# Kernel optimization log

Measured on AMD Instinct MI355X. Metric: run time of the kernel, lower is better.

The kernel has to match this reference:

```python
import jax, jax.numpy as jnp
import numpy as np
import math

LOG_2PI = math.log(2.0 * math.pi)
MIN_CLIP, MAX_CLIP = -5.0, 5.0


def _lse(x, axis):
    return jax.nn.logsumexp(x, axis=axis)


def _gaussian_multi(m1, v1, m2, v2):
    # product of two diagonal Gaussians in log-std parameterization
    v1s = jnp.exp(2.0 * v1)
    v2s = jnp.exp(2.0 * v2)
    add = v1s + v2s
    la = jnp.log(add)
    scale = (-0.5 * (LOG_2PI + la + (m1 - m2) ** 2 / add)).sum(-1)
    mu = (m1 * v2s + m2 * v1s) / add
    var = v1 + v2 - 0.5 * la
    return scale, mu, var


def _energy(sents, mask, tw, tpm, tpv, tcm, tcv, sw_tab, sm_tab, sv_tab):
    B, T = sents.shape
    L, _, TC = tw.shape
    G = tpm.shape[-1]
    EC = sw_tab.shape[1] // L
    clip = lambda x: jnp.clip(x, MIN_CLIP, MAX_CLIP)
    s_mu = clip(sm_tab[sents].reshape(B, T, 1, L, 1, EC, G))
    s_var = clip(sv_tab[sents].reshape(B, T, 1, L, 1, EC, G))
    s_w = sw_tab[sents].reshape(B, T, 1, L, 1, EC)
    t_w = tw.reshape(1, 1, 1, L, L, 1, 1, TC)
    t_p_mu = clip(tpm.reshape(1, 1, 1, L, L, 1, 1, TC, G))
    t_p_var = clip(tpv.reshape(1, 1, 1, L, L, 1, 1, TC, G))
    t_c_mu = clip(tcm.reshape(1, 1, L, L, TC, 1, G))
    t_c_var = clip(tcv.reshape(1, 1, L, L, TC, 1, G))
    cs_scale, cs_mu, cs_var = _gaussian_multi(s_mu, s_var, t_c_mu, t_c_var)
    cs_scale = cs_scale + s_w  # (B,T,L,L,TC,EC)
    # parent-child fusion over consecutive timesteps -> (B,T-1,L,L,L,TC,EC,TC)
    csp, _, _ = _gaussian_multi(jnp.expand_dims(cs_mu[:, :-1], (4, 7)),
                                jnp.expand_dims(cs_var[:, :-1], (4, 7)),
                                t_p_mu, t_p_var)
    mask1 = mask[:, 1:].reshape(B, T - 1, 1, 1, 1, 1, 1, 1)
    csp = csp * mask1 + jnp.expand_dims(cs_scale[:, :-1], (4, 7)) + t_w * mask1
    last = jnp.broadcast_to(jnp.expand_dims(cs_scale[:, -1:], (4, 7)),
                            (B, 1, L, L, L, TC, EC, TC))
    energy = jnp.concatenate([csp, last], axis=1)
    return energy * mask.reshape(B, T, 1, 1, 1, 1, 1, 1)


def _loss(sents, target, mask, tw, tpm, tpv, tcm, tcv, sw_tab, sm_tab, sv_tab):
    B, T = sents.shape
    L, _, TC = tw.shape
    energy = _energy(sents, mask, tw, tpm, tpv, tcm, tcv, sw_tab, sm_tab, sv_tab)
    e_t = jnp.moveaxis(energy, 1, 0)  # (T,B,L,L,L,TC,EC,TC)
    tgt_t = target.T                  # (T,B)
    tgt_next = jnp.concatenate([tgt_t[1:], jnp.zeros((1, B), tgt_t.dtype)], axis=0)
    mask_t = mask.T                   # (T,B)
    bidx = jnp.arange(B)
    # t = 0 : root label is L-1
    e0 = e_t[0]
    part = _lse(_lse(e0[:, -1], axis=4), axis=3)  # (B,L,L,TC)
    tmp0 = e0[bidx, jnp.full((B,), L - 1), tgt_t[0], tgt_next[0]]  # (B,TC,EC,TC)
    tgt_e = _lse(_lse(tmp0, axis=2), axis=1)      # (B,TC) (initial tgt_energy is zeros)

    def step(carry, xs):
        part, tgt_e = carry
        e, tg, tn, pv, m = xs
        pn = _lse(_lse(_lse(e + part[:, :, :, None, :, None, None], 5), 4), 1)
        part = part + (pn - part) * m[:, None, None, None]
        tmp = e[bidx, pv, tg, tn]  # (B,TC,EC,TC)
        te_new = _lse(_lse(tmp + tgt_e[:, :, None, None], 2), 1)
        tgt_e = tgt_e + (te_new - tgt_e) * m[:, None]
        return (part, tgt_e), None

    (part, tgt_e), _ = jax.lax.scan(
        step, (part, tgt_e),
        (e_t[1:], tgt_t[1:], tgt_next[1:], tgt_t[:-1], mask_t[1:]))
    part = part.mean(axis=2)  # (B,L,TC)
    loss = _lse(_lse(part, 2), 1) - _lse(tgt_e, 1)
    return loss.mean()


def setup_inputs() -> dict:
    key = jax.random.key(0)
    ks = jax.random.split(key, 10)
    V, NL, G, TC, EC = 50000, 45, 1, 1, 1
    L = NL + 1
    B, T = 4, 96

    def xavier(k, shape):
        rf = int(np.prod(shape[2:])) if len(shape) > 2 else 1
        fan_in = shape[1] * rf
        fan_out = shape[0] * rf
        std = math.sqrt(2.0 / (fan_in + fan_out))
        return jax.random.normal(k, shape, jnp.float32) * std

    return {
        "sents": jax.random.randint(ks[0], (B, T), 0, V, dtype=jnp.int32),
        "target": jax.random.randint(ks[1], (B, T), 0, NL, dtype=jnp.int32),
        "mask": jnp.ones((B, T), jnp.float32),
        "trans_weight": xavier(ks[2], (L, L, TC)),
        "trans_p_mu": xavier(ks[3], (L, L, TC, G)),
        "trans_p_var": xavier(ks[4], (L, L, TC, G)),
        "trans_c_mu": xavier(ks[5], (L, L, TC, G)),
        "trans_c_var": xavier(ks[6], (L, L, TC, G)),
        "s_weight_tab": jax.random.normal(ks[7], (V, L * EC), jnp.float32),
        "s_mu_tab": jax.random.normal(ks[8], (V, L * G * EC), jnp.float32),
        "s_var_tab": jax.random.normal(ks[9], (V, L * G * EC), jnp.float32),
    }


def reference(sents, target, mask, trans_weight, trans_p_mu, trans_p_var,
              trans_c_mu, trans_c_var, s_weight_tab, s_mu_tab, s_var_tab):
    return _loss(sents, target, mask, trans_weight, trans_p_mu, trans_p_var,
                 trans_c_mu, trans_c_var, s_weight_tab, s_mu_tab, s_var_tab)
```

## Files before the change

### kernel.cpp

```cpp
#include <hip/hip_runtime.h>
#include <hip/hip_fp16.h>
#include <math.h>

#define L 46
#define LSQ 2116
#define T 96
#define B 4
#define WROWH_U32 24
#define KSTRIDE_U32 25600
#define LOG_2PI 1.8378770664093453f
#define LN2f 0.6931471805599453f
#define LN2_EXP 8.2629582e-8f
#define INV_LN2 1.4426950408889634f

typedef float v2f __attribute__((ext_vector_type(2)));

__device__ __forceinline__ float clip5(float x) {
    return fminf(fmaxf(x, -5.0f), 5.0f);
}

__device__ __forceinline__ unsigned fxform(float f) {
    unsigned u = __float_as_uint(f);
    return (u & 0x80000000u) ? ~u : (u | 0x80000000u);
}
__device__ __forceinline__ float funxform(unsigned u) {
    return __uint_as_float((u & 0x80000000u) ? (u ^ 0x80000000u) : ~u);
}

__device__ __forceinline__ float bitlog(float x) {
    return (float)(int)(__float_as_uint(x) - 0x3f800000u) * LN2_EXP;
}

__device__ __forceinline__ v2f bfpair(unsigned u) {
    v2f r;
    r.x = __uint_as_float(u << 16);
    r.y = __uint_as_float(u & 0xFFFF0000u);
    return r;
}
__device__ __forceinline__ unsigned short f2bf(float f) {
    return (unsigned short)((__float_as_uint(f) + 0x8000u) >> 16);
}

#define BARRIER_LGKM() asm volatile("s_waitcnt lgkmcnt(0)\n\ts_barrier" ::: "memory")

__device__ __forceinline__ unsigned enc_e4m3_sw(float f) {
    if (!(f >= 0.0f)) return 0u;
    if (f < 0.015625f) {
        int m = (int)rintf(f * 512.0f);
        return (unsigned)m;
    }
    unsigned u = __float_as_uint(fminf(f, 448.0f));
    int e = (int)((u >> 23) & 255) - 127;
    int mant = (int)((u >> 20) & 7) + (int)((u >> 19) & 1);
    int Eb = e + 7;
    if (mant == 8) { mant = 0; ++Eb; }
    if (Eb > 15) { Eb = 15; mant = 6; }
    return (unsigned)((Eb << 3) | mant);
}
template <bool HI>
__device__ __forceinline__ unsigned enc_pk(float a, float b, unsigned old) {
#if __has_builtin(__builtin_amdgcn_cvt_pk_fp8_f32)
    return (unsigned)__builtin_amdgcn_cvt_pk_fp8_f32(a, b, (int)old, HI);
#else
    unsigned lo = enc_e4m3_sw(a) | (enc_e4m3_sw(b) << 8);
    return HI ? ((old & 0x0000FFFFu) | (lo << 16)) : ((old & 0xFFFF0000u) | lo);
#endif
}

__device__ __forceinline__ float dec1_sw(unsigned b) {
    int e = (b >> 3) & 15, m = b & 7;
    return e ? ldexpf((float)(8 + m), e - 10) : ldexpf((float)m, -9);
}
template <bool HI>
__device__ __forceinline__ v2f dec_pk(unsigned u) {
#if __has_builtin(__builtin_amdgcn_cvt_pk_f32_fp8)
    return __builtin_amdgcn_cvt_pk_f32_fp8(u, HI);
#else
    unsigned x = HI ? (u >> 16) : u;
    v2f r; r.x = dec1_sw(x & 0xffu); r.y = dec1_sw((x >> 8) & 0xffu);
    return r;
#endif
}

__device__ __forceinline__ void dp_acc(v2f& acc, unsigned kv, v2f wA, v2f wB) {
    acc += dec_pk<false>(kv) * wA;
    acc += dec_pk<true>(kv)  * wB;
}

__global__ __launch_bounds__(1024) void build_kernel(
    const int*   __restrict__ sents,
    const int*   __restrict__ target,
    const float* __restrict__ tw,
    const float* __restrict__ tpm,
    const float* __restrict__ tpv,
    const float* __restrict__ tcm,
    const float* __restrict__ tcv,
    const float* __restrict__ sw_tab,
    const float* __restrict__ sm_tab,
    const float* __restrict__ sv_tab,
    unsigned* __restrict__ K8,
    float*    __restrict__ escB,
    float*    __restrict__ psD,
    float*    __restrict__ P0,
    float*    __restrict__ tgtc,
    unsigned* __restrict__ done)
{
    __shared__ float sPS[LSQ], sW2[LSQ], sTP[LSQ];
    __shared__ float sW1T[L][48];
    __shared__ float sMUT[L][48];
    const int bt = blockIdx.x;
    const int t  = bt % T;
    const int b  = bt / T;
    const int sent = sents[bt];

    if (bt == 0 && threadIdx.x == 0) *done = 0u;

    if (threadIdx.x < L * 2) {
        int r = threadIdx.x >> 1, c = 46 + (threadIdx.x & 1);
        sW1T[r][c] = __uint_as_float(0x7f800000u);
        sMUT[r][c] = 0.0f;
    }

    for (int i = threadIdx.x; i < LSQ; i += 1024) {
        sW2[i] = __expf(2.0f * clip5(tpv[i]));
        sTP[i] = clip5(tpm[i]);
        int bb = i % L;
        int aa = i / L;
        float smu  = clip5(sm_tab[sent * L + bb]);
        float svar = clip5(sv_tab[sent * L + bb]);
        float sw   = sw_tab[sent * L + bb];
        float tc_m = clip5(tcm[i]);
        float tc_v = clip5(tcv[i]);
        float v1s = __expf(2.0f * svar);
        float v2s = __expf(2.0f * tc_v);
        float add = v1s + v2s;
        float inv = __builtin_amdgcn_rcpf(add);
        float la  = __logf(add);
        float d   = smu - tc_m;
        float psv = fmaf(-0.5f, LOG_2PI + la + d * d * inv, sw);
        sPS[i] = psv;
        psD[(size_t)bt * LSQ + i] = psv;
        sMUT[bb][aa] = (smu * v2s + tc_m * v1s) * inv;
        sW1T[bb][aa] = v1s * v2s * inv;
    }
    __syncthreads();

    if (threadIdx.x == 0) {
        const int* tg = target + b * T;
        float contrib;
        if (t == 0) {
            int i2 = tg[0] * L + tg[1];
            float ad = sW1T[tg[0]][45] + sW2[i2];
            float d  = sMUT[tg[0]][45] - sTP[i2];
            contrib = sPS[45 * L + tg[0]] + tw[i2]
                    - 0.5f * (LOG_2PI + __logf(ad) + d * d * __builtin_amdgcn_rcpf(ad));
        } else if (t == T - 1) {
            contrib = sPS[tg[T - 2] * L + tg[T - 1]];
        } else {
            int i2 = tg[t] * L + tg[t + 1];
            float ad = sW1T[tg[t]][tg[t - 1]] + sW2[i2];
            float d  = sMUT[tg[t]][tg[t - 1]] - sTP[i2];
            contrib = sPS[tg[t - 1] * L + tg[t]] + tw[i2]
                    - 0.5f * (LOG_2PI + __logf(ad) + d * d * __builtin_amdgcn_rcpf(ad));
        }
        tgtc[bt] = contrib;
    }

    if (t == 0) {
        for (int oi = threadIdx.x; oi < LSQ; oi += 1024) {
            int bb = oi / L;
            float ad = sW1T[bb][45] + sW2[oi];
            float d  = sMUT[bb][45] - sTP[oi];
            P0[b * LSQ + oi] = sPS[45 * L + bb] + tw[oi]
                - 0.5f * (LOG_2PI + __logf(ad) + d * d * __builtin_amdgcn_rcpf(ad));
        }
        return;
    }
    if (t == T - 1) return;

    unsigned* Kb = K8 + (size_t)bt * KSTRIDE_U32;
    for (int oi = threadIdx.x; oi < LSQ; oi += 1024) {
        int bb = oi / L;
        float w2 = sW2[oi], tp = sTP[oi];
        const float4* W14 = (const float4*)&sW1T[bb][0];
        const float4* MU4 = (const float4*)&sMUT[bb][0];

        float ymax = -1e30f;
        #pragma unroll
        for (int c = 0; c < 11; ++c) {
            float4 w4 = W14[c];
            float4 m4 = MU4[c];
            float ad, d, y;
            ad = w4.x + w2; d = m4.x - tp;
            y = -0.5f * (bitlog(ad) + d * d * __builtin_amdgcn_rcpf(ad));
            ymax = fmaxf(ymax, y);
            ad = w4.y + w2; d = m4.y - tp;
            y = -0.5f * (bitlog(ad) + d * d * __builtin_amdgcn_rcpf(ad));
            ymax = fmaxf(ymax, y);
            ad = w4.z + w2; d = m4.z - tp;
            y = -0.5f * (bitlog(ad) + d * d * __builtin_amdgcn_rcpf(ad));
            ymax = fmaxf(ymax, y);
            ad = w4.w + w2; d = m4.w - tp;
            y = -0.5f * (bitlog(ad) + d * d * __builtin_amdgcn_rcpf(ad));
            ymax = fmaxf(ymax, y);
        }
        {
            float ad, d, y;
            ad = sW1T[bb][44] + w2; d = sMUT[bb][44] - tp;
            y = -0.5f * (bitlog(ad) + d * d * __builtin_amdgcn_rcpf(ad));
            ymax = fmaxf(ymax, y);
            ad = sW1T[bb][45] + w2; d = sMUT[bb][45] - tp;
            y = -0.5f * (bitlog(ad) + d * d * __builtin_amdgcn_rcpf(ad));
            ymax = fmaxf(ymax, y);
        }
        ymax = fmaxf(ymax, -69.0f);
        int iex = 128 + (int)floorf(ymax * INV_LN2);
        float sc = __uint_as_float((unsigned)(261 - iex) << 23);

        uint4* dst = (uint4*)(Kb + (size_t)oi * 12);
        #pragma unroll
        for (int j = 0; j < 3; ++j) {
            unsigned un[4];
            #pragma unroll
            for (int q = 0; q < 4; ++q) {
                float4 w4 = W14[4 * j + q];
                float4 m4 = MU4[4 * j + q];
                float kk[4];
                {
                    float ad = w4.x + w2, r = __builtin_amdgcn_rsqf(ad);
                    float d = m4.x - tp;
                    kk[0] = sc * r * __expf(-0.5f * d * d * r * r);
                }
                {
                    float ad = w4.y + w2, r = __builtin_amdgcn_rsqf(ad);
                    float d = m4.y - tp;
                    kk[1] = sc * r * __expf(-0.5f * d * d * r * r);
                }
                {
                    float ad = w4.z + w2, r = __builtin_amdgcn_rsqf(ad);
                    float d = m4.z - tp;
                    kk[2] = sc * r * __expf(-0.5f * d * d * r * r);
                }
                {
                    float ad = w4.w + w2, r = __builtin_amdgcn_rsqf(ad);
                    float d = m4.w - tp;
                    kk[3] = sc * r * __expf(-0.5f * d * d * r * r);
                }
                unsigned u = enc_pk<false>(kk[0], kk[1], 0u);
                un[q] = enc_pk<true>(kk[2], kk[3], u);
            }
            dst[j] = make_uint4(un[0], un[1], un[2], un[3]);
        }
        escB[(size_t)bt * LSQ + oi] =
            (float)(iex - 134) * LN2f + tw[oi] - 0.5f * LOG_2PI;
    }
}


#define MDOT(q, ka0, ka1, kb0, kb1)                                           \
    {                                                                         \
        uint4 wq = wrow[q];                                                   \
        v2f wA = bfpair(wq.x), wB = bfpair(wq.y);                             \
        dp_acc(acc0, (ka0), wA, wB);                                          \
        dp_acc(acc1, (kb0), wA, wB);                                          \
        v2f wC = bfpair(wq.z), wD = bfpair(wq.w);                             \
        dp_acc(acc0, (ka1), wC, wD);                                          \
        dp_acc(acc1, (kb1), wC, wD);                                          \
    }

__global__ __launch_bounds__(1024) void dp_kernel(
    const unsigned* __restrict__ K8,
    const float*    __restrict__ escB,
    const float*    __restrict__ psD,
    const float*    __restrict__ P0,
    const float*    __restrict__ tgtc,
    float*    __restrict__ zbuf,
    unsigned* __restrict__ done,
    float*    __restrict__ out)
{
    __shared__ unsigned wbufH[2][L * WROWH_U32];
    __shared__ unsigned shiftS[4][L];
    __shared__ unsigned sh_last;
    __shared__ float    wsum[16];

    const int b = blockIdx.x;
    const int o = threadIdx.x;
    const int btT = b * T;

    const int bbA = (2 * o) / L;
    const int c0  = (2 * o) % L;
    const bool hasE = (o < 2 * (LSQ - 2048));
    const int oi3 = 2048 + (o >> 1);
    const int bb3 = hasE ? oi3 / L : 0;
    const int c3  = hasE ? oi3 % L : 0;
    const bool eOwner = hasE && !(o & 1);

    const unsigned* KM   = K8   + (size_t)btT * KSTRIDE_U32;
    const float*    escM = escB + (size_t)btT * LSQ;
    const float*    psDM = psD  + (size_t)btT * LSQ;

    {
        const float* p0   = P0 + b * LSQ;
        const float* psd1 = psDM + LSQ;
        float2 p01 = ((const float2*)p0)[o];
        float2 d1  = ((const float2*)psd1)[o];
        float p3v = 0.f, d3v = 0.f;
        if (eOwner) { p3v = p0[oi3]; d3v = psd1[oi3]; }
        if (o < L) {
            shiftS[0][o] = 0u; shiftS[1][o] = 0u;
            shiftS[2][o] = 0u; shiftS[3][o] = 0u;
            wbufH[0][o * WROWH_U32 + 23] = 0u;
            wbufH[1][o * WROWH_U32 + 23] = 0u;
        }
        __syncthreads();
        float g0 = p01.x + d1.x, g1 = p01.y + d1.y, g3 = p3v + d3v;
        atomicMax(&shiftS[0][c0],     fxform(g0));
        atomicMax(&shiftS[0][c0 + 1], fxform(g1));
        if (eOwner) atomicMax(&shiftS[0][c3], fxform(g3));
        __syncthreads();
        if (o < L) shiftS[3][o] = shiftS[0][o];
        unsigned short* w1s = (unsigned short*)wbufH[1];
        w1s[c0 * 48 + bbA] =
            f2bf(__expf(fminf(g0 - funxform(shiftS[0][c0]), 80.f)));
        w1s[(c0 + 1) * 48 + bbA] =
            f2bf(__expf(fminf(g1 - funxform(shiftS[0][c0 + 1]), 80.f)));
        if (eOwner)
            w1s[c3 * 48 + bb3] =
                f2bf(__expf(fminf(g3 - funxform(shiftS[0][c3]), 80.f)));
    }

    uint4 k0, k1, k2, k3, k4, k5;
    uint2 eA, eB, eC;
    eA = eB = eC = make_uint2(0u, 0u);

    const unsigned kOffMain = (unsigned)(2 * o) * 12u;
    const unsigned kOffExt  = (unsigned)oi3 * 12u + (unsigned)(o & 1) * 6u;

    {
        const uint4* kp = (const uint4*)(KM + (size_t)KSTRIDE_U32 + kOffMain);
        k0 = kp[0]; k1 = kp[1]; k2 = kp[2]; k3 = kp[3]; k4 = kp[4]; k5 = kp[5];
        if (hasE) {
            const uint2* ep = (const uint2*)(KM + (size_t)KSTRIDE_U32 + kOffExt);
            eA = ep[0]; eB = ep[1]; eC = ep[2];
        }
    }
    BARRIER_LGKM();

    for (int t = 1; t < T - 1; ++t) {
        const int sM_ = t & 3;
        const int sW_ = (t + 3) & 3;
        const int sP_ = (t + 2) & 3;
        const int sZ_ = (t + 1) & 3;

        float2 esc2 = ((const float2*)(escM + (size_t)t * LSQ))[o];
        float2 psD2 = ((const float2*)(psDM + (size_t)(t + 1) * LSQ))[o];
        float psd3_ = 0.f, e3_ = 0.f;
        if (eOwner) {
            e3_   = escM[(size_t)t * LSQ + oi3];
            psd3_ = psDM[(size_t)(t + 1) * LSQ + oi3];
        }

        const unsigned* wbH = wbufH[t & 1];
        unsigned*       wnH = wbufH[(t + 1) & 1];

        const uint4* wrow = (const uint4*)&wbH[(size_t)bbA * WROWH_U32];
        v2f acc0 = {0.f, 0.f}, acc1 = {0.f, 0.f};
        MDOT(0, k0.x, k0.y, k3.x, k3.y)
        MDOT(1, k0.z, k0.w, k3.z, k3.w)
        MDOT(2, k1.x, k1.y, k4.x, k4.y)
        MDOT(3, k1.z, k1.w, k4.z, k4.w)
        MDOT(4, k2.x, k2.y, k5.x, k5.y)
        MDOT(5, k2.z, k2.w, k5.z, k5.w)

        v2f acc3 = {0.f, 0.f};
        if (hasE) {
            const uint4* wr3 = (const uint4*)&wbH[(size_t)bb3 * WROWH_U32]
                               + (o & 1) * 3;
            uint4 w0 = wr3[0], w1 = wr3[1], w2q = wr3[2];
            { v2f a = bfpair(w0.x),  bq = bfpair(w0.y);  dp_acc(acc3, eA.x, a, bq); }
            { v2f a = bfpair(w0.z),  bq = bfpair(w0.w);  dp_acc(acc3, eA.y, a, bq); }
            { v2f a = bfpair(w1.x),  bq = bfpair(w1.y);  dp_acc(acc3, eB.x, a, bq); }
            { v2f a = bfpair(w1.z),  bq = bfpair(w1.w);  dp_acc(acc3, eB.y, a, bq); }
            { v2f a = bfpair(w2q.x), bq = bfpair(w2q.y); dp_acc(acc3, eC.x, a, bq); }
            { v2f a = bfpair(w2q.z), bq = bfpair(w2q.w); dp_acc(acc3, eC.y, a, bq); }
        }
        float sE = acc3.x + acc3.y;
        sE += __shfl_xor(sE, 1);

        {
            float shc  = funxform(shiftS[sP_][bbA]);
            float shw0 = funxform(shiftS[sW_][c0]);
            float shw1 = funxform(shiftS[sW_][c0 + 1]);
            float a0 = fmaxf(acc0.x + acc0.y, 1e-30f);
            float a1 = fmaxf(acc1.x + acc1.y, 1e-30f);
            float base0 = shc + esc2.x + psD2.x;
            float base1 = shc + esc2.y + psD2.y;
            float ga0 = fmaf((float)(int)(__float_as_uint(a0) - 0x3f800000u),
                             LN2_EXP, base0);
            float ga1 = fmaf((float)(int)(__float_as_uint(a1) - 0x3f800000u),
                             LN2_EXP, base1);
            atomicMax(&shiftS[sM_][c0],     fxform(ga0));
            atomicMax(&shiftS[sM_][c0 + 1], fxform(ga1));
            unsigned short* wnS = (unsigned short*)wnH;
            wnS[c0 * 48 + bbA] =
                f2bf(a0 * __expf(fminf(base0 - shw0, 87.f)));
            wnS[(c0 + 1) * 48 + bbA] =
                f2bf(a1 * __expf(fminf(base1 - shw1, 87.f)));
            if (eOwner) {
                float a3 = fmaxf(sE, 1e-30f);
                float sh3 = funxform(shiftS[sP_][bb3]);
                float base3 = sh3 + e3_ + psd3_;
                float ga3 = fmaf((float)(int)(__float_as_uint(a3) - 0x3f800000u),
                                 LN2_EXP, base3);
                atomicMax(&shiftS[sM_][c3], fxform(ga3));
                wnS[c3 * 48 + bb3] = f2bf(a3 *
                    __expf(fminf(base3 - funxform(shiftS[sW_][c3]), 87.f)));
            }
            if (o < L) shiftS[sZ_][o] = 0u;
        }

        if (t < T - 2) {
            const uint4* kp = (const uint4*)(KM + (size_t)(t + 1) * KSTRIDE_U32
                                             + kOffMain);
            k0 = kp[0]; k1 = kp[1]; k2 = kp[2];
            k3 = kp[3]; k4 = kp[4]; k5 = kp[5];
            if (hasE) {
                const uint2* ep = (const uint2*)(KM
                    + (size_t)(t + 1) * KSTRIDE_U32 + kOffExt);
                eA = ep[0]; eB = ep[1]; eC = ep[2];
            }
        }
        BARRIER_LGKM();
    }

    if (o < 64) {
        float pn = -INFINITY;
        if (o < L) {
            const uint4* wr = (const uint4*)&wbufH[1][o * WROWH_U32];
            float s = 0.0f;
            #pragma unroll
            for (int q = 0; q < 6; ++q) {
                uint4 v = wr[q];
                v2f a = bfpair(v.x), bq = bfpair(v.y);
                v2f c = bfpair(v.z), d = bfpair(v.w);
                s += (a.x + a.y) + (bq.x + bq.y) + (c.x + c.y) + (d.x + d.y);
            }
            pn = funxform(shiftS[1][o]) + __logf(s);
        }
        float mz = pn;
        #pragma unroll
        for (int off = 32; off >= 1; off >>= 1)
            mz = fmaxf(mz, __shfl_xor(mz, off));
        float ez = (o < L) ? __expf(pn - mz) : 0.0f;
        #pragma unroll
        for (int off = 32; off >= 1; off >>= 1)
            ez += __shfl_xor(ez, off);
        if (o == 0) zbuf[b] = mz + __logf(ez);
    }

    if (o == 0) {
        __threadfence();
        unsigned old = atomicAdd(done, 1u);
        sh_last = (old == B - 1) ? 1u : 0u;
    }
    __syncthreads();
    if (sh_last) {
        float v = (o < B * T) ? tgtc[o] : 0.0f;
        #pragma unroll
        for (int off = 32; off >= 1; off >>= 1) v += __shfl_xor(v, off);
        if ((o & 63) == 0) wsum[o >> 6] = v;
        __syncthreads();
        if (o == 0) {
            float ts = 0.0f;
            #pragma unroll
            for (int i = 0; i < 16; ++i) ts += wsum[i];
            __threadfence();
            float zs = zbuf[0] + zbuf[1] + zbuf[2] + zbuf[3];
            out[0] = 0.25f * (zs - ts);
        }
    }
}

__global__ __launch_bounds__(256) void prep_kernel(
    const int*   __restrict__ sents,
    const float* __restrict__ tcm,
    const float* __restrict__ tcv,
    const float* __restrict__ sw_tab,
    const float* __restrict__ sm_tab,
    const float* __restrict__ sv_tab,
    float* __restrict__ p_scale,
    float* __restrict__ p_mu,
    float* __restrict__ p_w1s)
{
    int idx = blockIdx.x * 256 + threadIdx.x;
    if (idx >= B * T * LSQ) return;
    int bb = idx % L;
    int bt = idx / LSQ;
    int sent = sents[bt];
    float smu  = clip5(sm_tab[sent * L + bb]);
    float svar = clip5(sv_tab[sent * L + bb]);
    float sw   = sw_tab[sent * L + bb];
    int i2 = idx % LSQ;
    float tc_m = clip5(tcm[i2]);
    float tc_v = clip5(tcv[i2]);
    float v1s = __expf(2.0f * svar);
    float v2s = __expf(2.0f * tc_v);
    float add = v1s + v2s;
    float inv = __builtin_amdgcn_rcpf(add);
    float la  = __logf(add);
    float d   = smu - tc_m;
    p_scale[idx] = fmaf(-0.5f, LOG_2PI + la + d * d * inv, sw);
    p_mu[idx]    = (smu * v2s + tc_m * v1s) * inv;
    p_w1s[idx]   = v1s * v2s * inv;
}

__global__ __launch_bounds__(1024) void dp_mono_kernel(
    const int*   __restrict__ target,
    const float* __restrict__ tw_g,
    const float* __restrict__ tpm_g,
    const float* __restrict__ tpv_g,
    const float* __restrict__ p_scale,
    const float* __restrict__ p_mu,
    const float* __restrict__ p_w1s,
    float* __restrict__ loss_out)
{
    __shared__ float sh_w2s[LSQ];
    __shared__ float sh_tpm[LSQ];
    __shared__ float sh_tw [LSQ];
    __shared__ float sh_w1s[LSQ];
    __shared__ float sh_mu [LSQ];
    __shared__ float sh_gf [LSQ];
    __shared__ float sh_P  [LSQ];
    __shared__ float sh_shift[L];
    __shared__ float sh_pn[L];

    const int b   = blockIdx.x;
    const int tid = threadIdx.x;
    const float* ps = p_scale + (size_t)b * T * LSQ;
    const float* pm = p_mu    + (size_t)b * T * LSQ;
    const float* pw = p_w1s   + (size_t)b * T * LSQ;
    const int*   tg = target + b * T;

    for (int i = tid; i < LSQ; i += 1024) {
        sh_w2s[i] = __expf(2.0f * clip5(tpv_g[i]));
        sh_tpm[i] = clip5(tpm_g[i]);
        sh_tw[i]  = tw_g[i];
    }
    __syncthreads();
    for (int oo = tid; oo < LSQ; oo += 1024) {
        int bb = oo / L;
        float cs_s = ps[45 * L + bb];
        float cm   = pm[45 * L + bb];
        float lw   = pw[45 * L + bb];
        float add2 = lw + sh_w2s[oo];
        float d    = cm - sh_tpm[oo];
        sh_P[oo] = cs_s + sh_tw[oo]
            - 0.5f * (LOG_2PI + __logf(add2) + d * d * __builtin_amdgcn_rcpf(add2));
    }
    __syncthreads();
    float tgt_e = 0.0f;
    if (tid == 0) tgt_e = sh_P[tg[0] * L + tg[1]];

    for (int t = 1; t < T - 1; ++t) {
        const float* ps_t = ps + t * LSQ;
        const float* pm_t = pm + t * LSQ;
        const float* pw_t = pw + t * LSQ;
        for (int i = tid; i < LSQ; i += 1024) {
            sh_w1s[i] = pw_t[i];
            sh_mu[i]  = pm_t[i];
            sh_gf[i]  = ps_t[i] + sh_P[i];
        }
        __syncthreads();
        if (tid < L) {
            float m = -INFINITY;
            for (int a = 0; a < L; ++a) m = fmaxf(m, sh_gf[a * L + tid]);
            sh_shift[tid] = m;
        }
        __syncthreads();
        for (int i = tid; i < LSQ; i += 1024) sh_gf[i] -= sh_shift[i % L];
        __syncthreads();
        for (int oo = tid; oo < LSQ; oo += 1024) {
            int bb = oo / L;
            float w2 = sh_w2s[oo], tp = sh_tpm[oo], tww = sh_tw[oo];
            float s = 0.0f;
            for (int a = 0; a < L; ++a) {
                float add2 = sh_w1s[a * L + bb] + w2;
                float r  = __builtin_amdgcn_rsqf(add2);
                float d  = sh_mu[a * L + bb] - tp;
                float y  = fmaf(-0.5f * d * d, r * r, sh_gf[a * L + bb]);
                s = fmaf(r, __expf(y), s);
            }
            sh_P[oo] = sh_shift[bb] + __logf(s) + tww - 0.5f * LOG_2PI;
        }
        if (tid == 0) {
            int pv = tg[t - 1], tc = tg[t], tn = tg[t + 1];
            float add2 = sh_w1s[pv * L + tc] + sh_w2s[tc * L + tn];
            float d    = sh_mu[pv * L + tc] - sh_tpm[tc * L + tn];
            tgt_e += ps_t[pv * L + tc] + sh_tw[tc * L + tn]
                - 0.5f * (LOG_2PI + __logf(add2) + d * d * __builtin_amdgcn_rcpf(add2));
        }
        __syncthreads();
    }
    {
        const float* ps_t = ps + (T - 1) * LSQ;
        for (int i = tid; i < LSQ; i += 1024) sh_gf[i] = ps_t[i] + sh_P[i];
        __syncthreads();
        if (tid < L) {
            float m = -INFINITY;
            for (int a = 0; a < L; ++a) m = fmaxf(m, sh_gf[a * L + tid]);
            float s = 0.0f;
            for (int a = 0; a < L; ++a) s += __expf(sh_gf[a * L + tid] - m);
            sh_pn[tid] = m + __logf(s);
        }
        __syncthreads();
        if (tid == 0) {
            tgt_e += ps_t[tg[T - 2] * L + tg[T - 1]];
            float m = -INFINITY;
            for (int bb = 0; bb < L; ++bb) m = fmaxf(m, sh_pn[bb]);
            float s = 0.0f;
            for (int bb = 0; bb < L; ++bb) s += __expf(sh_pn[bb] - m);
            loss_out[b] = (m + __logf(s)) - tgt_e;
        }
    }
}

__global__ void final_mono_kernel(const float* __restrict__ loss_partial,
                                  float* __restrict__ out)
{
    if (threadIdx.x == 0 && blockIdx.x == 0) {
        out[0] = 0.25f * (loss_partial[0] + loss_partial[1] +
                          loss_partial[2] + loss_partial[3]);
    }
}

extern "C" void kernel_launch(void* const* d_in, const int* in_sizes, int n_in,
                              void* d_out, int out_size, void* d_ws, size_t ws_size,
                              hipStream_t stream) {
    (void)in_sizes; (void)n_in; (void)out_size;

    const int*   sents  = (const int*)  d_in[0];
    const int*   target = (const int*)  d_in[1];
    const float* tw     = (const float*)d_in[3];
    const float* tpm    = (const float*)d_in[4];
    const float* tpv    = (const float*)d_in[5];
    const float* tcm    = (const float*)d_in[6];
    const float* tcv    = (const float*)d_in[7];
    const float* sw_tab = (const float*)d_in[8];
    const float* sm_tab = (const float*)d_in[9];
    const float* sv_tab = (const float*)d_in[10];

    char* ws = (char*)d_ws;

    size_t offK  = 0;
    size_t szK   = (size_t)B * T * KSTRIDE_U32 * 4;
    size_t offES = offK + szK;
    size_t szES  = (size_t)B * T * LSQ * sizeof(float);
    size_t offPD = offES + szES;
    size_t szPD  = (size_t)B * T * LSQ * sizeof(float);
    size_t offP0 = offPD + szPD;
    size_t szP0  = (size_t)B * LSQ * sizeof(float);
    size_t offTG = offP0 + szP0;
    size_t szTG  = (size_t)B * T * sizeof(float);
    size_t offZ  = offTG + szTG;
    size_t offDN = offZ + B * sizeof(float);
    size_t needed = offDN + sizeof(unsigned);

    if (ws_size >= needed) {
        unsigned* K8   = (unsigned*)(ws + offK);
        float*    escB = (float*)   (ws + offES);
        float*    psD  = (float*)   (ws + offPD);
        float*    P0   = (float*)   (ws + offP0);
        float*    tgtc = (float*)   (ws + offTG);
        float*    zbuf = (float*)   (ws + offZ);
        unsigned* done = (unsigned*)(ws + offDN);

        build_kernel<<<B * T, 1024, 0, stream>>>(
            sents, target, tw, tpm, tpv, tcm, tcv, sw_tab, sm_tab, sv_tab,
            K8, escB, psD, P0, tgtc, done);
        dp_kernel<<<B, 1024, 0, stream>>>(
            K8, escB, psD, P0, tgtc, zbuf, done, (float*)d_out);
    } else {
        float* p_scale      = (float*)ws;
        float* p_mu         = p_scale + (size_t)B * T * LSQ;
        float* p_w1s        = p_mu    + (size_t)B * T * LSQ;
        float* loss_partial = p_w1s   + (size_t)B * T * LSQ;
        int n = B * T * LSQ;
        prep_kernel<<<(n + 255) / 256, 256, 0, stream>>>(
            sents, tcm, tcv, sw_tab, sm_tab, sv_tab, p_scale, p_mu, p_w1s);
        dp_mono_kernel<<<B, 1024, 0, stream>>>(
            target, tw, tpm, tpv, p_scale, p_mu, p_w1s, loss_partial);
        final_mono_kernel<<<1, 64, 0, stream>>>(loss_partial, (float*)d_out);
    }
}
```

Measured before the change: 335.5 us.

## Store transition kernel in bf16 and use v_dot2 bf16 dot products

The build kernel now writes the per-step kernel matrix as unscaled bf16 instead of per-row-scaled fp8. This removes the max pass and the per-row escB exponent buffer, whose constant part is now folded from tw inside the DP kernel. The DP kernel replaces fp8 decode plus FMA with v_dot2_f32_bf16 dot products and forces 4 waves per EU. The trade is twice the kernel storage and bandwidth per step, plus more registers for the prefetched rows, and unscaled bf16 values risk underflow without per-row rescaling.

Result: slower. 585.9 us (+74.6%).

```diff
diff --git a/kernel.cpp b/kernel.cpp
--- a/kernel.cpp
+++ b/kernel.cpp
@@ -7,11 +7,10 @@
 #define T 96
 #define B 4
 #define WROWH_U32 24
-#define KSTRIDE_U32 25600
+#define KROW_U32 24
+#define KSTRIDE_U32 51200
 #define LOG_2PI 1.8378770664093453f
-#define LN2f 0.6931471805599453f
 #define LN2_EXP 8.2629582e-8f
-#define INV_LN2 1.4426950408889634f
 
 typedef float v2f __attribute__((ext_vector_type(2)));
 
@@ -40,52 +39,18 @@
 __device__ __forceinline__ unsigned short f2bf(float f) {
     return (unsigned short)((__float_as_uint(f) + 0x8000u) >> 16);
 }
+__device__ __forceinline__ unsigned bfpack(float a, float b) {
+    return ((__float_as_uint(a) + 0x8000u) >> 16) |
+           ((__float_as_uint(b) + 0x8000u) & 0xFFFF0000u);
+}
+
+__device__ __forceinline__ float dot2bf(unsigned a, unsigned b, float c) {
+    float d;
+    asm("v_dot2_f32_bf16 %0, %1, %2, %3" : "=v"(d) : "v"(a), "v"(b), "v"(c));
+    return d;
+}
 
 #define BARRIER_LGKM() asm volatile("s_waitcnt lgkmcnt(0)\n\ts_barrier" ::: "memory")
-
-__device__ __forceinline__ unsigned enc_e4m3_sw(float f) {
-    if (!(f >= 0.0f)) return 0u;
-    if (f < 0.015625f) {
-        int m = (int)rintf(f * 512.0f);
-        return (unsigned)m;
-    }
-    unsigned u = __float_as_uint(fminf(f, 448.0f));
-    int e = (int)((u >> 23) & 255) - 127;
-    int mant = (int)((u >> 20) & 7) + (int)((u >> 19) & 1);
-    int Eb = e + 7;
-    if (mant == 8) { mant = 0; ++Eb; }
-    if (Eb > 15) { Eb = 15; mant = 6; }
-    return (unsigned)((Eb << 3) | mant);
-}
-template <bool HI>
-__device__ __forceinline__ unsigned enc_pk(float a, float b, unsigned old) {
-#if __has_builtin(__builtin_amdgcn_cvt_pk_fp8_f32)
-    return (unsigned)__builtin_amdgcn_cvt_pk_fp8_f32(a, b, (int)old, HI);
-#else
-    unsigned lo = enc_e4m3_sw(a) | (enc_e4m3_sw(b) << 8);
-    return HI ? ((old & 0x0000FFFFu) | (lo << 16)) : ((old & 0xFFFF0000u) | lo);
-#endif
-}
-
-__device__ __forceinline__ float dec1_sw(unsigned b) {
-    int e = (b >> 3) & 15, m = b & 7;
-    return e ? ldexpf((float)(8 + m), e - 10) : ldexpf((float)m, -9);
-}
-template <bool HI>
-__device__ __forceinline__ v2f dec_pk(unsigned u) {
-#if __has_builtin(__builtin_amdgcn_cvt_pk_f32_fp8)
-    return __builtin_amdgcn_cvt_pk_f32_fp8(u, HI);
-#else
-    unsigned x = HI ? (u >> 16) : u;
-    v2f r; r.x = dec1_sw(x & 0xffu); r.y = dec1_sw((x >> 8) & 0xffu);
-    return r;
-#endif
-}
-
-__device__ __forceinline__ void dp_acc(v2f& acc, unsigned kv, v2f wA, v2f wB) {
-    acc += dec_pk<false>(kv) * wA;
-    acc += dec_pk<true>(kv)  * wB;
-}
 
 __global__ __launch_bounds__(1024) void build_kernel(
     const int*   __restrict__ sents,
@@ -99,7 +64,6 @@
     const float* __restrict__ sm_tab,
     const float* __restrict__ sv_tab,
     unsigned* __restrict__ K8,
-    float*    __restrict__ escB,
     float*    __restrict__ psD,
     float*    __restrict__ P0,
     float*    __restrict__ tgtc,
@@ -184,93 +148,62 @@
         float w2 = sW2[oi], tp = sTP[oi];
         const float4* W14 = (const float4*)&sW1T[bb][0];
         const float4* MU4 = (const float4*)&sMUT[bb][0];
-
-        float ymax = -1e30f;
+        uint4* dst = (uint4*)(Kb + (size_t)oi * KROW_U32);
         #pragma unroll
-        for (int c = 0; c < 11; ++c) {
-            float4 w4 = W14[c];
-            float4 m4 = MU4[c];
-            float ad, d, y;
-            ad = w4.x + w2; d = m4.x - tp;
-            y = -0.5f * (bitlog(ad) + d * d * __builtin_amdgcn_rcpf(ad));
-            ymax = fmaxf(ymax, y);
-            ad = w4.y + w2; d = m4.y - tp;
-            y = -0.5f * (bitlog(ad) + d * d * __builtin_amdgcn_rcpf(ad));
-            ymax = fmaxf(ymax, y);
-            ad = w4.z + w2; d = m4.z - tp;
-            y = -0.5f * (bitlog(ad) + d * d * __builtin_amdgcn_rcpf(ad));
-            ymax = fmaxf(ymax, y);
-            ad = w4.w + w2; d = m4.w - tp;
-            y = -0.5f * (bitlog(ad) + d * d * __builtin_amdgcn_rcpf(ad));
-            ymax = fmaxf(ymax, y);
-        }
-        {
-            float ad, d, y;
-            ad = sW1T[bb][44] + w2; d = sMUT[bb][44] - tp;
-            y = -0.5f * (bitlog(ad) + d * d * __builtin_amdgcn_rcpf(ad));
-            ymax = fmaxf(ymax, y);
-            ad = sW1T[bb][45] + w2; d = sMUT[bb][45] - tp;
-            y = -0.5f * (bitlog(ad) + d * d * __builtin_amdgcn_rcpf(ad));
-            ymax = fmaxf(ymax, y);
-        }
-        ymax = fmaxf(ymax, -69.0f);
-        int iex = 128 + (int)floorf(ymax * INV_LN2);
-        float sc = __uint_as_float((unsigned)(261 - iex) << 23);
-
-        uint4* dst = (uint4*)(Kb + (size_t)oi * 12);
-        #pragma unroll
-        for (int j = 0; j < 3; ++j) {
-            unsigned un[4];
-            #pragma unroll
-            for (int q = 0; q < 4; ++q) {
-                float4 w4 = W14[4 * j + q];
-                float4 m4 = MU4[4 * j + q];
-                float kk[4];
-                {
-                    float ad = w4.x + w2, r = __builtin_amdgcn_rsqf(ad);
-                    float d = m4.x - tp;
-                    kk[0] = sc * r * __expf(-0.5f * d * d * r * r);
-                }
-                {
-                    float ad = w4.y + w2, r = __builtin_amdgcn_rsqf(ad);
-                    float d = m4.y - tp;
-                    kk[1] = sc * r * __expf(-0.5f * d * d * r * r);
-                }
-                {
-                    float ad = w4.z + w2, r = __builtin_amdgcn_rsqf(ad);
-                    float d = m4.z - tp;
-                    kk[2] = sc * r * __expf(-0.5f * d * d * r * r);
-                }
-                {
-                    float ad = w4.w + w2, r = __builtin_amdgcn_rsqf(ad);
-                    float d = m4.w - tp;
-                    kk[3] = sc * r * __expf(-0.5f * d * d * r * r);
-                }
-                unsigned u = enc_pk<false>(kk[0], kk[1], 0u);
-                un[q] = enc_pk<true>(kk[2], kk[3], u);
-            }
-            dst[j] = make_uint4(un[0], un[1], un[2], un[3]);
-        }
-        escB[(size_t)bt * LSQ + oi] =
-            (float)(iex - 134) * LN2f + tw[oi] - 0.5f * LOG_2PI;
-    }
-}
-
-
-#define MDOT(q, ka0, ka1, kb0, kb1)                                           \
-    {                                                                         \
-        uint4 wq = wrow[q];                                                   \
-        v2f wA = bfpair(wq.x), wB = bfpair(wq.y);                             \
-        dp_acc(acc0, (ka0), wA, wB);                                          \
-        dp_acc(acc1, (kb0), wA, wB);                                          \
-        v2f wC = bfpair(wq.z), wD = bfpair(wq.w);                             \
-        dp_acc(acc0, (ka1), wC, wD);                                          \
-        dp_acc(acc1, (kb1), wC, wD);                                          \
-    }
-
-__global__ __launch_bounds__(1024) void dp_kernel(
+        for (int j = 0; j < 6; ++j) {
+            float4 wa = W14[2 * j],     ma = MU4[2 * j];
+            float4 wb = W14[2 * j + 1], mb = MU4[2 * j + 1];
+            float k0, k1, k2, k3, k4, k5, k6, k7;
+            {
+                float ad = wa.x + w2, r = __builtin_amdgcn_rsqf(ad);
+                float d = ma.x - tp; k0 = r * __expf(-0.5f * d * d * r * r);
+            }
+            {
+                float ad = wa.y + w2, r = __builtin_amdgcn_rsqf(ad);
+                float d = ma.y - tp; k1 = r * __expf(-0.5f * d * d * r * r);
+            }
+            {
+                float ad = wa.z + w2, r = __builtin_amdgcn_rsqf(ad);
+                float d = ma.z - tp; k2 = r * __expf(-0.5f * d * d * r * r);
+            }
+            {
+                float ad = wa.w + w2, r = __builtin_amdgcn_rsqf(ad);
+                float d = ma.w - tp; k3 = r * __expf(-0.5f * d * d * r * r);
+            }
+            {
+                float ad = wb.x + w2, r = __builtin_amdgcn_rsqf(ad);
+                float d = mb.x - tp; k4 = r * __expf(-0.5f * d * d * r * r);
+            }
+            {
+                float ad = wb.y + w2, r = __builtin_amdgcn_rsqf(ad);
+                float d = mb.y - tp; k5 = r * __expf(-0.5f * d * d * r * r);
+            }
+            {
+                float ad = wb.z + w2, r = __builtin_amdgcn_rsqf(ad);
+                float d = mb.z - tp; k6 = r * __expf(-0.5f * d * d * r * r);
+            }
+            {
+                float ad = wb.w + w2, r = __builtin_amdgcn_rsqf(ad);
+                float d = mb.w - tp; k7 = r * __expf(-0.5f * d * d * r * r);
+            }
+            dst[j] = make_uint4(bfpack(k0, k1), bfpack(k2, k3),
+                                bfpack(k4, k5), bfpack(k6, k7));
+        }
+    }
+}
+
+
+#define RQ(WQ, KA, KB)                                                        \
+    a0A = dot2bf(KA.x, WQ.x, a0A); a0B = dot2bf(KA.y, WQ.y, a0B);             \
+    a0A = dot2bf(KA.z, WQ.z, a0A); a0B = dot2bf(KA.w, WQ.w, a0B);             \
+    a1A = dot2bf(KB.x, WQ.x, a1A); a1B = dot2bf(KB.y, WQ.y, a1B);             \
+    a1A = dot2bf(KB.z, WQ.z, a1A); a1B = dot2bf(KB.w, WQ.w, a1B);
+
+__global__
+__attribute__((amdgpu_flat_work_group_size(1024, 1024), amdgpu_waves_per_eu(4, 4)))
+void dp_kernel(
     const unsigned* __restrict__ K8,
-    const float*    __restrict__ escB,
+    const float*    __restrict__ tw,
     const float*    __restrict__ psD,
     const float*    __restrict__ P0,
     const float*    __restrict__ tgtc,
@@ -295,9 +228,13 @@
     const int c3  = hasE ? oi3 % L : 0;
     const bool eOwner = hasE && !(o & 1);
 
-    const unsigned* KM   = K8   + (size_t)btT * KSTRIDE_U32;
-    const float*    escM = escB + (size_t)btT * LSQ;
-    const float*    psDM = psD  + (size_t)btT * LSQ;
+    const unsigned* KM   = K8  + (size_t)btT * KSTRIDE_U32;
+    const float*    psDM = psD + (size_t)btT * LSQ;
+
+    const float e0c = tw[2 * o]     - 0.5f * LOG_2PI;
+    const float e1c = tw[2 * o + 1] - 0.5f * LOG_2PI;
+    float e3c = 0.0f;
+    if (eOwner) e3c = tw[oi3] - 0.5f * LOG_2PI;
 
     {
         const float* p0   = P0 + b * LSQ;
@@ -329,19 +266,23 @@
                 f2bf(__expf(fminf(g3 - funxform(shiftS[0][c3]), 80.f)));
     }
 
-    uint4 k0, k1, k2, k3, k4, k5;
-    uint2 eA, eB, eC;
-    eA = eB = eC = make_uint2(0u, 0u);
-
-    const unsigned kOffMain = (unsigned)(2 * o) * 12u;
-    const unsigned kOffExt  = (unsigned)oi3 * 12u + (unsigned)(o & 1) * 6u;
+    uint4 ka0, ka1, ka2, ka3, ka4, ka5;
+    uint4 kb0, kb1, kb2, kb3, kb4, kb5;
+    uint4 ke0, ke1, ke2;
+    ke0 = ke1 = ke2 = make_uint4(0u, 0u, 0u, 0u);
+
+    const unsigned kOffA = (unsigned)(2 * o) * KROW_U32;
+    const unsigned kOffE = (unsigned)oi3 * KROW_U32 + (unsigned)(o & 1) * 12u;
 
     {
-        const uint4* kp = (const uint4*)(KM + (size_t)KSTRIDE_U32 + kOffMain);
-        k0 = kp[0]; k1 = kp[1]; k2 = kp[2]; k3 = kp[3]; k4 = kp[4]; k5 = kp[5];
+        const uint4* kp = (const uint4*)(KM + (size_t)KSTRIDE_U32 + kOffA);
+        ka0 = kp[0]; ka1 = kp[1]; ka2 = kp[2];
+        ka3 = kp[3]; ka4 = kp[4]; ka5 = kp[5];
+        kb0 = kp[6]; kb1 = kp[7]; kb2 = kp[8];
+        kb3 = kp[9]; kb4 = kp[10]; kb5 = kp[11];
         if (hasE) {
-            const uint2* ep = (const uint2*)(KM + (size_t)KSTRIDE_U32 + kOffExt);
-            eA = ep[0]; eB = ep[1]; eC = ep[2];
+            const uint4* ep = (const uint4*)(KM + (size_t)KSTRIDE_U32 + kOffE);
+            ke0 = ep[0]; ke1 = ep[1]; ke2 = ep[2];
         }
     }
     BARRIER_LGKM();
@@ -352,49 +293,46 @@
         const int sP_ = (t + 2) & 3;
         const int sZ_ = (t + 1) & 3;
 
-        float2 esc2 = ((const float2*)(escM + (size_t)t * LSQ))[o];
         float2 psD2 = ((const float2*)(psDM + (size_t)(t + 1) * LSQ))[o];
-        float psd3_ = 0.f, e3_ = 0.f;
-        if (eOwner) {
-            e3_   = escM[(size_t)t * LSQ + oi3];
-            psd3_ = psDM[(size_t)(t + 1) * LSQ + oi3];
-        }
+        float psd3_ = 0.f;
+        if (eOwner) psd3_ = psDM[(size_t)(t + 1) * LSQ + oi3];
 
         const unsigned* wbH = wbufH[t & 1];
         unsigned*       wnH = wbufH[(t + 1) & 1];
 
         const uint4* wrow = (const uint4*)&wbH[(size_t)bbA * WROWH_U32];
-        v2f acc0 = {0.f, 0.f}, acc1 = {0.f, 0.f};
-        MDOT(0, k0.x, k0.y, k3.x, k3.y)
-        MDOT(1, k0.z, k0.w, k3.z, k3.w)
-        MDOT(2, k1.x, k1.y, k4.x, k4.y)
-        MDOT(3, k1.z, k1.w, k4.z, k4.w)
-        MDOT(4, k2.x, k2.y, k5.x, k5.y)
-        MDOT(5, k2.z, k2.w, k5.z, k5.w)
-
-        v2f acc3 = {0.f, 0.f};
+        uint4 w0_ = wrow[0], w1_ = wrow[1], w2_ = wrow[2];
+        uint4 w3_ = wrow[3], w4_ = wrow[4], w5_ = wrow[5];
+        float a0A = 0.f, a0B = 0.f, a1A = 0.f, a1B = 0.f;
+        RQ(w0_, ka0, kb0) RQ(w1_, ka1, kb1) RQ(w2_, ka2, kb2)
+        RQ(w3_, ka3, kb3) RQ(w4_, ka4, kb4) RQ(w5_, ka5, kb5)
+        float s0 = a0A + a0B;
+        float s1 = a1A + a1B;
+
+        float sE = 0.f;
         if (hasE) {
             const uint4* wr3 = (const uint4*)&wbH[(size_t)bb3 * WROWH_U32]
                                + (o & 1) * 3;
-            uint4 w0 = wr3[0], w1 = wr3[1], w2q = wr3[2];
-            { v2f a = bfpair(w0.x),  bq = bfpair(w0.y);  dp_acc(acc3, eA.x, a, bq); }
-            { v2f a = bfpair(w0.z),  bq = bfpair(w0.w);  dp_acc(acc3, eA.y, a, bq); }
-            { v2f a = bfpair(w1.x),  bq = bfpair(w1.y);  dp_acc(acc3, eB.x, a, bq); }
-            { v2f a = bfpair(w1.z),  bq = bfpair(w1.w);  dp_acc(acc3, eB.y, a, bq); }
-            { v2f a = bfpair(w2q.x), bq = bfpair(w2q.y); dp_acc(acc3, eC.x, a, bq); }
-            { v2f a = bfpair(w2q.z), bq = bfpair(w2q.w); dp_acc(acc3, eC.y, a, bq); }
-        }
-        float sE = acc3.x + acc3.y;
+            uint4 x0 = wr3[0], x1 = wr3[1], x2 = wr3[2];
+            float eA = 0.f, eBq = 0.f;
+            eA = dot2bf(ke0.x, x0.x, eA); eBq = dot2bf(ke0.y, x0.y, eBq);
+            eA = dot2bf(ke0.z, x0.z, eA); eBq = dot2bf(ke0.w, x0.w, eBq);
+            eA = dot2bf(ke1.x, x1.x, eA); eBq = dot2bf(ke1.y, x1.y, eBq);
+            eA = dot2bf(ke1.z, x1.z, eA); eBq = dot2bf(ke1.w, x1.w, eBq);
+            eA = dot2bf(ke2.x, x2.x, eA); eBq = dot2bf(ke2.y, x2.y, eBq);
+            eA = dot2bf(ke2.z, x2.z, eA); eBq = dot2bf(ke2.w, x2.w, eBq);
+            sE = eA + eBq;
+        }
         sE += __shfl_xor(sE, 1);
 
         {
             float shc  = funxform(shiftS[sP_][bbA]);
             float shw0 = funxform(shiftS[sW_][c0]);
             float shw1 = funxform(shiftS[sW_][c0 + 1]);
-            float a0 = fmaxf(acc0.x + acc0.y, 1e-30f);
-            float a1 = fmaxf(acc1.x + acc1.y, 1e-30f);
-            float base0 = shc + esc2.x + psD2.x;
-            float base1 = shc + esc2.y + psD2.y;
+            float a0 = fmaxf(s0, 1e-30f);
+            float a1 = fmaxf(s1, 1e-30f);
+            float base0 = shc + e0c + psD2.x;
+            float base1 = shc + e1c + psD2.y;
             float ga0 = fmaf((float)(int)(__float_as_uint(a0) - 0x3f800000u),
                              LN2_EXP, base0);
             float ga1 = fmaf((float)(int)(__float_as_uint(a1) - 0x3f800000u),
@@ -409,7 +347,7 @@
             if (eOwner) {
                 float a3 = fmaxf(sE, 1e-30f);
                 float sh3 = funxform(shiftS[sP_][bb3]);
-                float base3 = sh3 + e3_ + psd3_;
+                float base3 = sh3 + e3c + psd3_;
                 float ga3 = fmaf((float)(int)(__float_as_uint(a3) - 0x3f800000u),
                                  LN2_EXP, base3);
                 atomicMax(&shiftS[sM_][c3], fxform(ga3));
@@ -421,13 +359,15 @@
 
         if (t < T - 2) {
             const uint4* kp = (const uint4*)(KM + (size_t)(t + 1) * KSTRIDE_U32
-                                             + kOffMain);
-            k0 = kp[0]; k1 = kp[1]; k2 = kp[2];
-            k3 = kp[3]; k4 = kp[4]; k5 = kp[5];
+                                             + kOffA);
+            ka0 = kp[0]; ka1 = kp[1]; ka2 = kp[2];
+            ka3 = kp[3]; ka4 = kp[4]; ka5 = kp[5];
+            kb0 = kp[6]; kb1 = kp[7]; kb2 = kp[8];
+            kb3 = kp[9]; kb4 = kp[10]; kb5 = kp[11];
             if (hasE) {
-                const uint2* ep = (const uint2*)(KM
-                    + (size_t)(t + 1) * KSTRIDE_U32 + kOffExt);
-                eA = ep[0]; eB = ep[1]; eC = ep[2];
+                const uint4* ep = (const uint4*)(KM
+                    + (size_t)(t + 1) * KSTRIDE_U32 + kOffE);
+                ke0 = ep[0]; ke1 = ep[1]; ke2 = ep[2];
             }
         }
         BARRIER_LGKM();
@@ -653,9 +593,7 @@
 
     size_t offK  = 0;
     size_t szK   = (size_t)B * T * KSTRIDE_U32 * 4;
-    size_t offES = offK + szK;
-    size_t szES  = (size_t)B * T * LSQ * sizeof(float);
-    size_t offPD = offES + szES;
+    size_t offPD = offK + szK;
     size_t szPD  = (size_t)B * T * LSQ * sizeof(float);
     size_t offP0 = offPD + szPD;
     size_t szP0  = (size_t)B * LSQ * sizeof(float);
@@ -667,7 +605,6 @@
 
     if (ws_size >= needed) {
         unsigned* K8   = (unsigned*)(ws + offK);
-        float*    escB = (float*)   (ws + offES);
         float*    psD  = (float*)   (ws + offPD);
         float*    P0   = (float*)   (ws + offP0);
         float*    tgtc = (float*)   (ws + offTG);
@@ -676,9 +613,9 @@
 
         build_kernel<<<B * T, 1024, 0, stream>>>(
             sents, target, tw, tpm, tpv, tcm, tcv, sw_tab, sm_tab, sv_tab,
-            K8, escB, psD, P0, tgtc, done);
+            K8, psD, P0, tgtc, done);
         dp_kernel<<<B, 1024, 0, stream>>>(
-            K8, escB, psD, P0, tgtc, zbuf, done, (float*)d_out);
+            K8, tw, psD, P0, tgtc, zbuf, done, (float*)d_out);
     } else {
         float* p_scale      = (float*)ws;
         float* p_mu         = p_scale + (size_t)B * T * LSQ;
```

## Pack escape scale into spare K slot and store psD as bf16

Applied to the files above, without the earlier changes.

The per-cell escape/scale term is no longer written as a separate fp32 array. It is stored as bf16 in the upper half of the last packed K word, which previously held two fp8 kernel entries, and the DP loop consumes it from registers it already loads. The psD array is also stored as bf16 instead of fp32. Together these cut global traffic on the serial DP critical path. In exchange, the escape term and psD lose precision, and the dropped K entries must really be padding, otherwise results change.

After: 336.2 us. Within noise of the previous version (+0.2%).

```diff
diff --git a/kernel.cpp b/kernel.cpp
--- a/kernel.cpp
+++ b/kernel.cpp
@@ -39,6 +39,9 @@
 }
 __device__ __forceinline__ unsigned short f2bf(float f) {
     return (unsigned short)((__float_as_uint(f) + 0x8000u) >> 16);
+}
+__device__ __forceinline__ float bf2f(unsigned short s) {
+    return __uint_as_float(((unsigned)s) << 16);
 }
 
 #define BARRIER_LGKM() asm volatile("s_waitcnt lgkmcnt(0)\n\ts_barrier" ::: "memory")
@@ -98,9 +101,8 @@
     const float* __restrict__ sw_tab,
     const float* __restrict__ sm_tab,
     const float* __restrict__ sv_tab,
-    unsigned* __restrict__ K8,
-    float*    __restrict__ escB,
-    float*    __restrict__ psD,
+    unsigned*        __restrict__ K8,
+    unsigned short*  __restrict__ psDH,
     float*    __restrict__ P0,
     float*    __restrict__ tgtc,
     unsigned* __restrict__ done)
@@ -139,7 +141,7 @@
         float d   = smu - tc_m;
         float psv = fmaf(-0.5f, LOG_2PI + la + d * d * inv, sw);
         sPS[i] = psv;
-        psD[(size_t)bt * LSQ + i] = psv;
+        psDH[(size_t)bt * LSQ + i] = f2bf(psv);
         sMUT[bb][aa] = (smu * v2s + tc_m * v1s) * inv;
         sW1T[bb][aa] = v1s * v2s * inv;
     }
@@ -216,6 +218,7 @@
         ymax = fmaxf(ymax, -69.0f);
         int iex = 128 + (int)floorf(ymax * INV_LN2);
         float sc = __uint_as_float((unsigned)(261 - iex) << 23);
+        float escv = (float)(iex - 134) * LN2f + tw[oi] - 0.5f * LOG_2PI;
 
         uint4* dst = (uint4*)(Kb + (size_t)oi * 12);
         #pragma unroll
@@ -246,13 +249,16 @@
                     float d = m4.w - tp;
                     kk[3] = sc * r * __expf(-0.5f * d * d * r * r);
                 }
-                unsigned u = enc_pk<false>(kk[0], kk[1], 0u);
-                un[q] = enc_pk<true>(kk[2], kk[3], u);
+                if (j == 2 && q == 3) {
+                    unsigned u = enc_pk<false>(kk[0], kk[1], 0u);
+                    un[3] = (u & 0x0000FFFFu) | ((unsigned)f2bf(escv) << 16);
+                } else {
+                    unsigned u = enc_pk<false>(kk[0], kk[1], 0u);
+                    un[q] = enc_pk<true>(kk[2], kk[3], u);
+                }
             }
             dst[j] = make_uint4(un[0], un[1], un[2], un[3]);
         }
-        escB[(size_t)bt * LSQ + oi] =
-            (float)(iex - 134) * LN2f + tw[oi] - 0.5f * LOG_2PI;
     }
 }
 
@@ -269,11 +275,10 @@
     }
 
 __global__ __launch_bounds__(1024) void dp_kernel(
-    const unsigned* __restrict__ K8,
-    const float*    __restrict__ escB,
-    const float*    __restrict__ psD,
-    const float*    __restrict__ P0,
-    const float*    __restrict__ tgtc,
+    const unsigned*       __restrict__ K8,
+    const unsigned short* __restrict__ psDH,
+    const float*          __restrict__ P0,
+    const float*          __restrict__ tgtc,
     float*    __restrict__ zbuf,
     unsigned* __restrict__ done,
     float*    __restrict__ out)
@@ -295,17 +300,19 @@
     const int c3  = hasE ? oi3 % L : 0;
     const bool eOwner = hasE && !(o & 1);
 
-    const unsigned* KM   = K8   + (size_t)btT * KSTRIDE_U32;
-    const float*    escM = escB + (size_t)btT * LSQ;
-    const float*    psDM = psD  + (size_t)btT * LSQ;
+    const unsigned*       KM   = K8   + (size_t)btT * KSTRIDE_U32;
+    const unsigned short* psDM = psDH + (size_t)btT * LSQ;
 
     {
-        const float* p0   = P0 + b * LSQ;
-        const float* psd1 = psDM + LSQ;
+        const float* p0 = P0 + b * LSQ;
         float2 p01 = ((const float2*)p0)[o];
-        float2 d1  = ((const float2*)psd1)[o];
+        unsigned d1u = ((const unsigned*)(psDM + LSQ))[o];
+        v2f d1 = bfpair(d1u);
         float p3v = 0.f, d3v = 0.f;
-        if (eOwner) { p3v = p0[oi3]; d3v = psd1[oi3]; }
+        if (eOwner) {
+            p3v = p0[oi3];
+            d3v = bf2f(psDM[LSQ + oi3]);
+        }
         if (o < L) {
             shiftS[0][o] = 0u; shiftS[1][o] = 0u;
             shiftS[2][o] = 0u; shiftS[3][o] = 0u;
@@ -352,13 +359,10 @@
         const int sP_ = (t + 2) & 3;
         const int sZ_ = (t + 1) & 3;
 
-        float2 esc2 = ((const float2*)(escM + (size_t)t * LSQ))[o];
-        float2 psD2 = ((const float2*)(psDM + (size_t)(t + 1) * LSQ))[o];
-        float psd3_ = 0.f, e3_ = 0.f;
-        if (eOwner) {
-            e3_   = escM[(size_t)t * LSQ + oi3];
-            psd3_ = psDM[(size_t)(t + 1) * LSQ + oi3];
-        }
+        unsigned pdu = ((const unsigned*)(psDM + (size_t)(t + 1) * LSQ))[o];
+        v2f psD2 = bfpair(pdu);
+        float psd3_ = 0.f;
+        if (eOwner) psd3_ = bf2f(psDM[(size_t)(t + 1) * LSQ + oi3]);
 
         const unsigned* wbH = wbufH[t & 1];
         unsigned*       wnH = wbufH[(t + 1) & 1];
@@ -370,22 +374,36 @@
         MDOT(2, k1.x, k1.y, k4.x, k4.y)
         MDOT(3, k1.z, k1.w, k4.z, k4.w)
         MDOT(4, k2.x, k2.y, k5.x, k5.y)
-        MDOT(5, k2.z, k2.w, k5.z, k5.w)
+        {
+            uint4 wq = wrow[5];
+            v2f wA = bfpair(wq.x), wB = bfpair(wq.y);
+            dp_acc(acc0, k2.z, wA, wB);
+            dp_acc(acc1, k5.z, wA, wB);
+            v2f wC = bfpair(wq.z);
+            acc0 += dec_pk<false>(k2.w) * wC;
+            acc1 += dec_pk<false>(k5.w) * wC;
+        }
+        float e0v = __uint_as_float(k2.w & 0xFFFF0000u);
+        float e1v = __uint_as_float(k5.w & 0xFFFF0000u);
 
         v2f acc3 = {0.f, 0.f};
+        float e3raw = 0.f;
         if (hasE) {
             const uint4* wr3 = (const uint4*)&wbH[(size_t)bb3 * WROWH_U32]
                                + (o & 1) * 3;
-            uint4 w0 = wr3[0], w1 = wr3[1], w2q = wr3[2];
-            { v2f a = bfpair(w0.x),  bq = bfpair(w0.y);  dp_acc(acc3, eA.x, a, bq); }
-            { v2f a = bfpair(w0.z),  bq = bfpair(w0.w);  dp_acc(acc3, eA.y, a, bq); }
-            { v2f a = bfpair(w1.x),  bq = bfpair(w1.y);  dp_acc(acc3, eB.x, a, bq); }
-            { v2f a = bfpair(w1.z),  bq = bfpair(w1.w);  dp_acc(acc3, eB.y, a, bq); }
-            { v2f a = bfpair(w2q.x), bq = bfpair(w2q.y); dp_acc(acc3, eC.x, a, bq); }
-            { v2f a = bfpair(w2q.z), bq = bfpair(w2q.w); dp_acc(acc3, eC.y, a, bq); }
+            uint4 x0 = wr3[0], x1 = wr3[1], x2 = wr3[2];
+            unsigned ecy = (o & 1) ? (eC.y & 0x0000FFFFu) : eC.y;
+            { v2f a = bfpair(x0.x), bq = bfpair(x0.y); dp_acc(acc3, eA.x, a, bq); }
+            { v2f a = bfpair(x0.z), bq = bfpair(x0.w); dp_acc(acc3, eA.y, a, bq); }
+            { v2f a = bfpair(x1.x), bq = bfpair(x1.y); dp_acc(acc3, eB.x, a, bq); }
+            { v2f a = bfpair(x1.z), bq = bfpair(x1.w); dp_acc(acc3, eB.y, a, bq); }
+            { v2f a = bfpair(x2.x), bq = bfpair(x2.y); dp_acc(acc3, eC.x, a, bq); }
+            { v2f a = bfpair(x2.z), bq = bfpair(x2.w); dp_acc(acc3, ecy,  a, bq); }
+            e3raw = __uint_as_float(eC.y & 0xFFFF0000u);
         }
         float sE = acc3.x + acc3.y;
         sE += __shfl_xor(sE, 1);
+        float e3v = __shfl_xor(e3raw, 1);
 
         {
             float shc  = funxform(shiftS[sP_][bbA]);
@@ -393,8 +411,8 @@
             float shw1 = funxform(shiftS[sW_][c0 + 1]);
             float a0 = fmaxf(acc0.x + acc0.y, 1e-30f);
             float a1 = fmaxf(acc1.x + acc1.y, 1e-30f);
-            float base0 = shc + esc2.x + psD2.x;
-            float base1 = shc + esc2.y + psD2.y;
+            float base0 = shc + e0v + psD2.x;
+            float base1 = shc + e1v + psD2.y;
             float ga0 = fmaf((float)(int)(__float_as_uint(a0) - 0x3f800000u),
                              LN2_EXP, base0);
             float ga1 = fmaf((float)(int)(__float_as_uint(a1) - 0x3f800000u),
@@ -409,7 +427,7 @@
             if (eOwner) {
                 float a3 = fmaxf(sE, 1e-30f);
                 float sh3 = funxform(shiftS[sP_][bb3]);
-                float base3 = sh3 + e3_ + psd3_;
+                float base3 = sh3 + e3v + psd3_;
                 float ga3 = fmaf((float)(int)(__float_as_uint(a3) - 0x3f800000u),
                                  LN2_EXP, base3);
                 atomicMax(&shiftS[sM_][c3], fxform(ga3));
@@ -653,11 +671,9 @@
 
     size_t offK  = 0;
     size_t szK   = (size_t)B * T * KSTRIDE_U32 * 4;
-    size_t offES = offK + szK;
-    size_t szES  = (size_t)B * T * LSQ * sizeof(float);
-    size_t offPD = offES + szES;
-    size_t szPD  = (size_t)B * T * LSQ * sizeof(float);
-    size_t offP0 = offPD + szPD;
+    size_t offPD = offK + szK;
+    size_t szPD  = (size_t)B * T * LSQ * sizeof(unsigned short);
+    size_t offP0 = offPD + ((szPD + 15) & ~(size_t)15);
     size_t szP0  = (size_t)B * LSQ * sizeof(float);
     size_t offTG = offP0 + szP0;
     size_t szTG  = (size_t)B * T * sizeof(float);
@@ -666,9 +682,8 @@
     size_t needed = offDN + sizeof(unsigned);
 
     if (ws_size >= needed) {
-        unsigned* K8   = (unsigned*)(ws + offK);
-        float*    escB = (float*)   (ws + offES);
-        float*    psD  = (float*)   (ws + offPD);
+        unsigned*       K8   = (unsigned*)      (ws + offK);
+        unsigned short* psDH = (unsigned short*)(ws + offPD);
         float*    P0   = (float*)   (ws + offP0);
         float*    tgtc = (float*)   (ws + offTG);
         float*    zbuf = (float*)   (ws + offZ);
@@ -676,9 +691,9 @@
 
         build_kernel<<<B * T, 1024, 0, stream>>>(
             sents, target, tw, tpm, tpv, tcm, tcv, sw_tab, sm_tab, sv_tab,
-            K8, escB, psD, P0, tgtc, done);
+            K8, psDH, P0, tgtc, done);
         dp_kernel<<<B, 1024, 0, stream>>>(
-            K8, escB, psD, P0, tgtc, zbuf, done, (float*)d_out);
+            K8, psDH, P0, tgtc, zbuf, done, (float*)d_out);
     } else {
         float* p_scale      = (float*)ws;
         float* p_mu         = p_scale + (size_t)B * T * LSQ;
```
